# Optimization experiments

Hardware: AMD Instinct MI355X
Metric: run time of the kernel (lower is better)

The kernel has to match this reference:

```python
import jax, jax.numpy as jnp
import numpy as np

B, S, H, T = 64, 512, 768, 400


def setup_inputs() -> dict:
    key = jax.random.key(0)
    k1, k2 = jax.random.split(key)
    hidden = jax.random.normal(k1, (B, S, H), dtype=jnp.float32)
    # word_ids: non-decreasing piece->word map per sample, like HF tokenizer word_ids()
    word_ids = jnp.sort(jax.random.randint(k2, (B, S), 0, T), axis=-1).astype(jnp.int32)
    return {"hidden": hidden, "word_ids": word_ids, "num_tokens": T}


def reference(hidden, word_ids, num_tokens):
    # Ragged segment mean-pool: pool subword pieces into per-word reps.
    # hidden: [B, S, H] float; word_ids: [B, S] int in [0, num_tokens)
    b, s, h = hidden.shape
    # Flatten (sample, word) into one global segment id: sample*T + word
    seg = (jnp.arange(b, dtype=word_ids.dtype)[:, None] * num_tokens + word_ids).reshape(-1)
    sums = jax.ops.segment_sum(hidden.reshape(b * s, h), seg, num_segments=b * num_tokens)
    counts = jax.ops.segment_sum(jnp.ones((b * s,), hidden.dtype), seg, num_segments=b * num_tokens)
    # Words with zero pieces -> sum 0 / 1 = 0, matching torch.zeros fallback
    pooled = sums / jnp.maximum(counts, 1.0)[:, None]
    return pooled.reshape(b, num_tokens, h)
```

## Files before the change

### kernel.cpp

```cpp
#include <hip/hip_runtime.h>


#define BB 64
#define SS 512
#define HH 768
#define TT 400
#define NF4 (HH / 4)
#define W   20
#define WGB (TT / W)
#define NTHR 192
#define CH  8

__global__ __launch_bounds__(NTHR) void bert_lattice_pool_kernel(
    const float* __restrict__ hidden,
    const int* __restrict__ word_ids,
    float* __restrict__ out)
{
    const int blk = blockIdx.x;
    const int b   = blk / WGB;
    const int w0  = (blk - b * WGB) * W;

    __shared__ int s_w[SS];
    __shared__ int s_bnd[W + 1];

    const int tid = threadIdx.x;

    const int2* wrow2 = reinterpret_cast<const int2*>(word_ids + b * SS);
    reinterpret_cast<int2*>(s_w)[tid] = wrow2[tid];
    if (tid < 64) reinterpret_cast<int2*>(s_w)[NTHR + tid] = wrow2[NTHR + tid];
    if (tid <= W) s_bnd[tid] = SS;
    __syncthreads();

    for (int s = tid; s < SS; s += NTHR) {
        const int w  = s_w[s];
        const int wp = (s == 0) ? -1 : s_w[s - 1];
        int lo = wp + 1; if (lo < w0) lo = w0;
        int hi = w;      if (hi > w0 + W) hi = w0 + W;
        for (int t = lo; t <= hi; ++t) s_bnd[t - w0] = s;
    }
    __syncthreads();

    const int wv   = tid >> 6;
    const int lane = tid & 63;

    const int r0 = s_bnd[0];
    const int r1 = s_bnd[W];

    const float4* hp = reinterpret_cast<const float4*>(hidden)
                       + (size_t)b * SS * NF4 + wv * 64 + lane;
    float4* op = reinterpret_cast<float4*>(out)
                 + ((size_t)b * TT + w0) * NF4 + wv * 64 + lane;

    const float4 z4 = make_float4(0.f, 0.f, 0.f, 0.f);

    int t = 0;
    while (t < W && s_bnd[t + 1] == r0) { op[(size_t)t * NF4] = z4; ++t; }
    if (r0 >= r1) return;

    int ws = r0;
    int e  = (t < W) ? s_bnd[t + 1] : -1;
    float4 acc = z4;
    const int rmax = r1 - 1;

#define LOADC(Bufr, base)                                             \
    _Pragma("unroll")                                                 \
    for (int i = 0; i < CH; ++i) {                                    \
        int rr = (base) + i;                                          \
        rr = rr > rmax ? rmax : rr;       \
        Bufr[i] = hp[(size_t)rr * NF4];                               \
    }

#define PROC(Bufr, base)                                              \
    _Pragma("unroll")                                                 \
    for (int i = 0; i < CH; ++i) {                                    \
        const int rI = (base) + i;     \
        if (rI < r1) {                                                \
            acc.x += Bufr[i].x; acc.y += Bufr[i].y;                   \
            acc.z += Bufr[i].z; acc.w += Bufr[i].w;                   \
            if (rI + 1 == e) {                                        \
                const int cnt = e - ws;                               \
                const float inv = 1.0f / (float)cnt;                  \
                op[(size_t)t * NF4] = make_float4(acc.x * inv,        \
                    acc.y * inv, acc.z * inv, acc.w * inv);           \
                acc = z4; ws = e; ++t;                                \
                while (t < W && s_bnd[t + 1] == e) {                  \
                    op[(size_t)t * NF4] = z4; ++t;    \
                }                                                     \
                e = (t < W) ? s_bnd[t + 1] : -1;                      \
            }                                                         \
        }                                                             \
    }

    float4 A[CH], Bf[CH];
    int r = r0;
    LOADC(A, r);
    for (;;) {
        LOADC(Bf, r + CH);
        PROC(A, r);
        r += CH;
        if (r >= r1) break;
        LOADC(A, r + CH);
        PROC(Bf, r);
        r += CH;
        if (r >= r1) break;
    }

#undef LOADC
#undef PROC
}

extern "C" void kernel_launch(void* const* d_in, const int* in_sizes, int n_in,
                              void* d_out, int out_size, void* d_ws, size_t ws_size,
                              hipStream_t stream) {
    (void)in_sizes; (void)n_in; (void)d_ws; (void)ws_size; (void)out_size;
    const float* hidden   = (const float*)d_in[0];
    const int*   word_ids = (const int*)d_in[1];
    float*       out      = (float*)d_out;

    dim3 grid(BB * WGB);
    dim3 block(NTHR);
    bert_lattice_pool_kernel<<<grid, block, 0, stream>>>(hidden, word_ids, out);
}
```

Baseline: 178.0 us.

## Stage hidden rows into LDS via async global_load_lds double buffering

Replaces per-thread float4 register prefetch with direct global-to-LDS DMA loads (global_load_lds, 16 bytes per lane) into a double-buffered shared tile of 8 rows, synchronized with vmcnt waits and block barriers. The block grows from 192 to 256 threads, and each thread now accumulates 3 scalar columns read from LDS. The goal is to keep more loads in flight without spending registers. It adds about 48KB of LDS per block, which may lower occupancy, plus two barriers per chunk, and the scalar output stores are strided across the row.

```diff
diff --git a/kernel.cpp b/kernel.cpp
--- a/kernel.cpp
+++ b/kernel.cpp
@@ -1,17 +1,23 @@
 #include <hip/hip_runtime.h>
+#include <stdint.h>
 
 
 #define BB 64
 #define SS 512
 #define HH 768
 #define TT 400
-#define NF4 (HH / 4)
 #define W   20
 #define WGB (TT / W)
-#define NTHR 192
 #define CH  8
 
-__global__ __launch_bounds__(NTHR) void bert_lattice_pool_kernel(
+__device__ __forceinline__ void dma16(const float* g, const float* l) {
+    __builtin_amdgcn_global_load_lds(
+        (const __attribute__((address_space(1))) void*)(uintptr_t)g,
+        (__attribute__((address_space(3))) void*)(uint32_t)(uintptr_t)l,
+        16 , 0, 0);
+}
+
+__global__ __launch_bounds__(256) void bert_lattice_pool_kernel(
     const float* __restrict__ hidden,
     const int* __restrict__ word_ids,
     float* __restrict__ out)
@@ -20,18 +26,20 @@
     const int b   = blk / WGB;
     const int w0  = (blk - b * WGB) * W;
 
-    __shared__ int s_w[SS];
-    __shared__ int s_bnd[W + 1];
+    __shared__ float s_rows[2 * CH * HH];
+    __shared__ int   s_w[SS];
+    __shared__ int   s_bnd[W + 1];
 
-    const int tid = threadIdx.x;
+    const int tid  = threadIdx.x;
+    const int wv   = tid >> 6;
+    const int lane = tid & 63;
 
     const int2* wrow2 = reinterpret_cast<const int2*>(word_ids + b * SS);
     reinterpret_cast<int2*>(s_w)[tid] = wrow2[tid];
-    if (tid < 64) reinterpret_cast<int2*>(s_w)[NTHR + tid] = wrow2[NTHR + tid];
     if (tid <= W) s_bnd[tid] = SS;
     __syncthreads();
 
-    for (int s = tid; s < SS; s += NTHR) {
+    for (int s = tid; s < SS; s += 256) {
         const int w  = s_w[s];
         const int wp = (s == 0) ? -1 : s_w[s - 1];
         int lo = wp + 1; if (lo < w0) lo = w0;
@@ -40,73 +48,82 @@
     }
     __syncthreads();
 
-    const int wv   = tid >> 6;
-    const int lane = tid & 63;
-
     const int r0 = s_bnd[0];
     const int r1 = s_bnd[W];
 
-    const float4* hp = reinterpret_cast<const float4*>(hidden)
-                       + (size_t)b * SS * NF4 + wv * 64 + lane;
-    float4* op = reinterpret_cast<float4*>(out)
-                 + ((size_t)b * TT + w0) * NF4 + wv * 64 + lane;
+    float* outp = out + (size_t)b * TT * HH;
 
-    const float4 z4 = make_float4(0.f, 0.f, 0.f, 0.f);
+#define ZWORD(tt) do {                                                \
+        float* o_ = outp + (size_t)(w0 + (tt)) * HH + tid;            \
+        o_[0] = 0.f; o_[256] = 0.f; o_[512] = 0.f;                    \
+    } while (0)
+
+    if (r0 >= r1) {
+        for (int t = 0; t < W; ++t) ZWORD(t);
+        return;
+    }
 
     int t = 0;
-    while (t < W && s_bnd[t + 1] == r0) { op[(size_t)t * NF4] = z4; ++t; }
-    if (r0 >= r1) return;
+    while (t < W && s_bnd[t + 1] == r0) { ZWORD(t); ++t; }
 
     int ws = r0;
     int e  = (t < W) ? s_bnd[t + 1] : -1;
-    float4 acc = z4;
+    float a0 = 0.f, a1 = 0.f, a2 = 0.f;
+
     const int rmax = r1 - 1;
+    const int nch  = (r1 - r0 + CH - 1) / CH;
+    const float* hsrc = hidden + (size_t)b * SS * HH;
 
-#define LOADC(Bufr, base)                                             \
-    _Pragma("unroll")                                                 \
-    for (int i = 0; i < CH; ++i) {                                    \
-        int rr = (base) + i;                                          \
-        rr = rr > rmax ? rmax : rr;       \
-        Bufr[i] = hp[(size_t)rr * NF4];                               \
+    auto STAGE = [&](int c) {
+        const int cbase = r0 + c * CH;
+        const float* lb = s_rows + (c & 1) * (CH * HH);
+        #pragma unroll
+        for (int k = 0; k < 6; ++k) {
+            const int rrow = wv * 2 + k / 3;
+            const int seg  = (k % 3) * 256;
+            int rr = cbase + rrow;
+            rr = rr > rmax ? rmax : rr;
+            dma16(hsrc + (size_t)rr * HH + seg + lane * 4,
+                  lb + rrow * HH + seg);
+        }
+    };
+
+    STAGE(0);
+    if (nch > 1) STAGE(1);
+
+    for (int c = 0; c < nch; ++c) {
+        if (c + 1 < nch) { asm volatile("s_waitcnt vmcnt(6)" ::: "memory"); }
+        else             { asm volatile("s_waitcnt vmcnt(0)" ::: "memory"); }
+        __builtin_amdgcn_sched_barrier(0);
+        __builtin_amdgcn_s_barrier();
+        __builtin_amdgcn_sched_barrier(0);
+
+        const int cbase = r0 + c * CH;
+        const float* lb = s_rows + (c & 1) * (CH * HH) + tid;
+        #pragma unroll
+        for (int i = 0; i < CH; ++i) {
+            const int r = cbase + i;
+            if (r < r1) {
+                a0 += lb[i * HH];
+                a1 += lb[i * HH + 256];
+                a2 += lb[i * HH + 512];
+                if (r + 1 == e) {
+                    const float inv = 1.0f / (float)(e - ws);
+                    float* o = outp + (size_t)(w0 + t) * HH + tid;
+                    o[0] = a0 * inv; o[256] = a1 * inv; o[512] = a2 * inv;
+                    a0 = a1 = a2 = 0.f; ws = e; ++t;
+                    while (t < W && s_bnd[t + 1] == e) { ZWORD(t); ++t; }
+                    e = (t < W) ? s_bnd[t + 1] : -1;
+                }
+            }
+        }
+
+        __builtin_amdgcn_sched_barrier(0);
+        __builtin_amdgcn_s_barrier();
+        __builtin_amdgcn_sched_barrier(0);
+        if (c + 2 < nch) STAGE(c + 2);
     }
-
-#define PROC(Bufr, base)                                              \
-    _Pragma("unroll")                                                 \
-    for (int i = 0; i < CH; ++i) {                                    \
-        const int rI = (base) + i;     \
-        if (rI < r1) {                                                \
-            acc.x += Bufr[i].x; acc.y += Bufr[i].y;                   \
-            acc.z += Bufr[i].z; acc.w += Bufr[i].w;                   \
-            if (rI + 1 == e) {                                        \
-                const int cnt = e - ws;                               \
-                const float inv = 1.0f / (float)cnt;                  \
-                op[(size_t)t * NF4] = make_float4(acc.x * inv,        \
-                    acc.y * inv, acc.z * inv, acc.w * inv);           \
-                acc = z4; ws = e; ++t;                                \
-                while (t < W && s_bnd[t + 1] == e) {                  \
-                    op[(size_t)t * NF4] = z4; ++t;    \
-                }                                                     \
-                e = (t < W) ? s_bnd[t + 1] : -1;                      \
-            }                                                         \
-        }                                                             \
-    }
-
-    float4 A[CH], Bf[CH];
-    int r = r0;
-    LOADC(A, r);
-    for (;;) {
-        LOADC(Bf, r + CH);
-        PROC(A, r);
-        r += CH;
-        if (r >= r1) break;
-        LOADC(A, r + CH);
-        PROC(Bf, r);
-        r += CH;
-        if (r >= r1) break;
-    }
-
-#undef LOADC
-#undef PROC
+#undef ZWORD
 }
 
 extern "C" void kernel_launch(void* const* d_in, const int* in_sizes, int n_in,
@@ -118,6 +135,6 @@
     float*       out      = (float*)d_out;
 
     dim3 grid(BB * WGB);
-    dim3 block(NTHR);
+    dim3 block(256);
     bert_lattice_pool_kernel<<<grid, block, 0, stream>>>(hidden, word_ids, out);
 }
```

After: 177.7 us. Within noise of the previous version (-0.2%).
